# Kernel optimization log

Measured on AMD Instinct MI355X. Metric: run time of the kernel, lower is better.

The kernel has to match this reference:

```python
import jax, jax.numpy as jnp
import numpy as np

D_MODEL = 2048
NUM_EXPERTS = 64
TOP_K = 2
N_TOKENS = 16384


def setup_inputs() -> dict:
    key = jax.random.key(0)
    kx, kw = jax.random.split(key)
    x = jax.random.normal(kx, (N_TOKENS, D_MODEL), dtype=jnp.float32)
    # match nn.Linear default init scale roughly (not bit-exact; math is what matters)
    W = jax.random.normal(kw, (D_MODEL, NUM_EXPERTS), dtype=jnp.float32) * (1.0 / np.sqrt(D_MODEL))
    b = jnp.zeros((NUM_EXPERTS,), dtype=jnp.float32)
    return {"x": x, "W": W, "b": b}


def reference(x, W, b):
    # eval-mode forward (self.training False => no noise)
    logits = jnp.einsum("td,de->te", x, W) + b          # [T, E]
    weights = jax.nn.softmax(logits, axis=-1)             # [T, E]
    topk_weights, topk_indices = jax.lax.top_k(weights, TOP_K)  # [T, k] each
    return topk_weights, topk_indices, weights
```

## Files before the change

kernel.cpp:

```cpp
#include <hip/hip_runtime.h>
#include <math.h>


#define T_TOK 16384
#define DMOD  2048
#define NEXP  64
#define TM    64
#define BK    64
#define NCH   (DMOD / BK)
#define NT    512
#define LDK   72

typedef __attribute__((ext_vector_type(8))) short short8;
typedef __attribute__((ext_vector_type(4))) float f32x4;

__device__ __forceinline__ unsigned short bf16_rne(float f) {
  unsigned int u = __float_as_uint(f);
  unsigned int r = (u + 0x7fffu + ((u >> 16) & 1u)) >> 16;
  return (unsigned short)r;
}
__device__ __forceinline__ float bf16_up(unsigned short h) {
  return __uint_as_float(((unsigned int)h) << 16);
}
__device__ __forceinline__ void split3(float v, unsigned short& h,
                                       unsigned short& m, unsigned short& l) {
  h = bf16_rne(v);
  const float e1 = v - bf16_up(h);
  m = bf16_rne(e1);
  const float e2 = e1 - bf16_up(m);
  l = bf16_rne(e2);
}

__global__ __launch_bounds__(NT, 4) void gating_kernel(
    const float* __restrict__ x, const float* __restrict__ W,
    const float* __restrict__ bias, float* __restrict__ out) {
  __shared__ __align__(16) unsigned short smem[6 * TM * LDK];
  unsigned short* xs_h = smem;
  unsigned short* xs_m = smem + TM * LDK;
  unsigned short* xs_l = smem + 2 * TM * LDK;
  unsigned short* wt_h = smem + 3 * TM * LDK;
  unsigned short* wt_m = smem + 4 * TM * LDK;
  unsigned short* wt_l = smem + 5 * TM * LDK;
  float* lg    = (float*)smem;
  float* red_m = (float*)smem + 4160;
  float* red_s = (float*)smem + 4224;

  const int tid = threadIdx.x;
  const int l   = tid & 63;
  const int w   = tid >> 6;
  const int q   = l >> 4;
  const int c   = l & 15;
  const int t0  = blockIdx.x * TM;

  const int xtok = tid >> 3;
  const int xk0  = (tid & 7) * 8;
  const int wn0  = (tid & 31) * 2;
  const int wk0  = (tid >> 5) * 4;
  const float* xg = x + (size_t)(t0 + xtok) * DMOD + xk0;
  const float* wg = W + (size_t)wk0 * NEXP + wn0;

  const int arow = (w & 3) * 16 + c;
  const int bn0  = (w >> 2) * 32 + c;
  const unsigned short* pa_h = xs_h + arow * LDK + q * 8;
  const unsigned short* pa_m = xs_m + arow * LDK + q * 8;
  const unsigned short* pa_l = xs_l + arow * LDK + q * 8;
  const unsigned short* pb_h = wt_h + bn0 * LDK + q * 8;
  const unsigned short* pb_m = wt_m + bn0 * LDK + q * 8;
  const unsigned short* pb_l = wt_l + bn0 * LDK + q * 8;

  f32x4 acc0 = {0.f, 0.f, 0.f, 0.f};
  f32x4 acc1 = {0.f, 0.f, 0.f, 0.f};

  float4 pxa, pxb;
  float2 pwv[4];
  pxa = *(const float4*)(xg);
  pxb = *(const float4*)(xg + 4);
#pragma unroll
  for (int i = 0; i < 4; ++i) pwv[i] = *(const float2*)(wg + (size_t)i * NEXP);

  for (int k = 0; k < NCH; ++k) {
    {
      float xv[8] = {pxa.x, pxa.y, pxa.z, pxa.w, pxb.x, pxb.y, pxb.z, pxb.w};
      unsigned short h[8], m[8], lo[8];
#pragma unroll
      for (int j = 0; j < 8; ++j) split3(xv[j], h[j], m[j], lo[j]);
      uint4 hp, mp, lp;
      hp.x = (unsigned)h[0] | ((unsigned)h[1] << 16);
      hp.y = (unsigned)h[2] | ((unsigned)h[3] << 16);
      hp.z = (unsigned)h[4] | ((unsigned)h[5] << 16);
      hp.w = (unsigned)h[6] | ((unsigned)h[7] << 16);
      mp.x = (unsigned)m[0] | ((unsigned)m[1] << 16);
      mp.y = (unsigned)m[2] | ((unsigned)m[3] << 16);
      mp.z = (unsigned)m[4] | ((unsigned)m[5] << 16);
      mp.w = (unsigned)m[6] | ((unsigned)m[7] << 16);
      lp.x = (unsigned)lo[0] | ((unsigned)lo[1] << 16);
      lp.y = (unsigned)lo[2] | ((unsigned)lo[3] << 16);
      lp.z = (unsigned)lo[4] | ((unsigned)lo[5] << 16);
      lp.w = (unsigned)lo[6] | ((unsigned)lo[7] << 16);
      *(uint4*)(xs_h + xtok * LDK + xk0) = hp;
      *(uint4*)(xs_m + xtok * LDK + xk0) = mp;
      *(uint4*)(xs_l + xtok * LDK + xk0) = lp;
#pragma unroll
      for (int n = 0; n < 2; ++n) {
        unsigned short wh[4], wm[4], wl[4];
#pragma unroll
        for (int i = 0; i < 4; ++i) {
          const float v = n == 0 ? pwv[i].x : pwv[i].y;
          split3(v, wh[i], wm[i], wl[i]);
        }
        uint2 hp2, mp2, lp2;
        hp2.x = (unsigned)wh[0] | ((unsigned)wh[1] << 16);
        hp2.y = (unsigned)wh[2] | ((unsigned)wh[3] << 16);
        mp2.x = (unsigned)wm[0] | ((unsigned)wm[1] << 16);
        mp2.y = (unsigned)wm[2] | ((unsigned)wm[3] << 16);
        lp2.x = (unsigned)wl[0] | ((unsigned)wl[1] << 16);
        lp2.y = (unsigned)wl[2] | ((unsigned)wl[3] << 16);
        *(uint2*)(wt_h + (wn0 + n) * LDK + wk0) = hp2;
        *(uint2*)(wt_m + (wn0 + n) * LDK + wk0) = mp2;
        *(uint2*)(wt_l + (wn0 + n) * LDK + wk0) = lp2;
      }
    }
    __syncthreads();

    if (k + 1 < NCH) {
      const int kc = (k + 1) * BK;
      pxa = *(const float4*)(xg + kc);
      pxb = *(const float4*)(xg + kc + 4);
#pragma unroll
      for (int i = 0; i < 4; ++i)
        pwv[i] = *(const float2*)(wg + (size_t)(kc + i) * NEXP);
    }

#pragma unroll
    for (int s = 0; s < 2; ++s) {
      const int ko = s * 32;
      const short8 a_h = *(const short8*)(pa_h + ko);
      const short8 a_m = *(const short8*)(pa_m + ko);
      const short8 a_l = *(const short8*)(pa_l + ko);
      const short8 b_h0 = *(const short8*)(pb_h + ko);
      const short8 b_m0 = *(const short8*)(pb_m + ko);
      const short8 b_l0 = *(const short8*)(pb_l + ko);
      const short8 b_h1 = *(const short8*)(pb_h + 16 * LDK + ko);
      const short8 b_m1 = *(const short8*)(pb_m + 16 * LDK + ko);
      const short8 b_l1 = *(const short8*)(pb_l + 16 * LDK + ko);
      acc0 = __builtin_amdgcn_mfma_f32_16x16x32_bf16(a_h, b_h0, acc0, 0, 0, 0);
      acc0 = __builtin_amdgcn_mfma_f32_16x16x32_bf16(a_h, b_m0, acc0, 0, 0, 0);
      acc0 = __builtin_amdgcn_mfma_f32_16x16x32_bf16(a_m, b_h0, acc0, 0, 0, 0);
      acc0 = __builtin_amdgcn_mfma_f32_16x16x32_bf16(a_m, b_m0, acc0, 0, 0, 0);
      acc0 = __builtin_amdgcn_mfma_f32_16x16x32_bf16(a_h, b_l0, acc0, 0, 0, 0);
      acc0 = __builtin_amdgcn_mfma_f32_16x16x32_bf16(a_l, b_h0, acc0, 0, 0, 0);
      acc1 = __builtin_amdgcn_mfma_f32_16x16x32_bf16(a_h, b_h1, acc1, 0, 0, 0);
      acc1 = __builtin_amdgcn_mfma_f32_16x16x32_bf16(a_h, b_m1, acc1, 0, 0, 0);
      acc1 = __builtin_amdgcn_mfma_f32_16x16x32_bf16(a_m, b_h1, acc1, 0, 0, 0);
      acc1 = __builtin_amdgcn_mfma_f32_16x16x32_bf16(a_m, b_m1, acc1, 0, 0, 0);
      acc1 = __builtin_amdgcn_mfma_f32_16x16x32_bf16(a_h, b_l1, acc1, 0, 0, 0);
      acc1 = __builtin_amdgcn_mfma_f32_16x16x32_bf16(a_l, b_h1, acc1, 0, 0, 0);
    }
    __syncthreads();
  }

  {
    const int row0 = (w & 3) * 16 + q * 4;
    const int e0 = (w >> 2) * 32 + c;
    const float bv0 = bias[e0];
    const float bv1 = bias[e0 + 16];
#pragma unroll
    for (int r = 0; r < 4; ++r) {
      lg[(row0 + r) * 65 + e0] = acc0[r] + bv0;
      lg[(row0 + r) * 65 + e0 + 16] = acc1[r] + bv1;
    }
  }
  __syncthreads();

  if (tid < TM) {
    float mx = -INFINITY;
    for (int e = 0; e < NEXP; ++e) mx = fmaxf(mx, lg[tid * 65 + e]);
    float sum = 0.f, b1 = -INFINITY, b2 = -INFINITY;
    int i1 = 0, i2 = 0;
    for (int e = 0; e < NEXP; ++e) {
      const float v = lg[tid * 65 + e];
      sum += expf(v - mx);
      if (v > b1) {
        b2 = b1; i2 = i1; b1 = v; i1 = e;
      } else if (v > b2) {
        b2 = v; i2 = e;
      }
    }
    const float inv = 1.f / sum;
    const int t = t0 + tid;
    out[2 * t + 0] = expf(b1 - mx) * inv;
    out[2 * t + 1] = expf(b2 - mx) * inv;
    out[2 * T_TOK + 2 * t + 0] = (float)i1;
    out[2 * T_TOK + 2 * t + 1] = (float)i2;
    red_m[tid] = mx;
    red_s[tid] = inv;
  }
  __syncthreads();

#pragma unroll
  for (int r = 0; r < (TM * NEXP) / NT; ++r) {
    const int idx = r * NT + tid;
    const int tt = idx >> 6;
    const int e = idx & 63;
    out[4 * T_TOK + (size_t)(t0 + tt) * NEXP + e] =
        expf(lg[tt * 65 + e] - red_m[tt]) * red_s[tt];
  }
}

extern "C" void kernel_launch(void* const* d_in, const int* in_sizes, int n_in,
                              void* d_out, int out_size, void* d_ws, size_t ws_size,
                              hipStream_t stream) {
  const float* x = (const float*)d_in[0];
  const float* W = (const float*)d_in[1];
  const float* b = (const float*)d_in[2];
  float* out = (float*)d_out;
  gating_kernel<<<dim3(T_TOK / TM), dim3(NT), 0, stream>>>(x, W, b, out);
}
```

Baseline: 227.1 us.

## Pre-split W into MFMA fragments and use single-wave blocks without LDS staging

Adds a pre-pass kernel that splits W into bf16 hi/mid/lo parts once, stored in workspace in MFMA fragment order. The gating kernel becomes one wavefront per 16 tokens, reading x straight from global memory into registers and loading B fragments from the prepacked buffer with register double buffering. This removes the per-chunk LDS staging, the barriers and the redundant split of W in every block. In exchange there is an extra launch, heavy register pressure from the prefetch arrays, and W fragments are re-read from L2 by every block. The softmax and top-2 are now split across 4 lanes per token with shuffle reductions.

```diff
diff --git a/kernel.cpp b/kernel.cpp
--- a/kernel.cpp
+++ b/kernel.cpp
@@ -5,14 +5,12 @@
 #define T_TOK 16384
 #define DMOD  2048
 #define NEXP  64
-#define TM    64
-#define BK    64
-#define NCH   (DMOD / BK)
-#define NT    512
-#define LDK   72
+#define NKS   64
 
 typedef __attribute__((ext_vector_type(8))) short short8;
 typedef __attribute__((ext_vector_type(4))) float f32x4;
+
+#define MFMA16 __builtin_amdgcn_mfma_f32_16x16x32_bf16
 
 __device__ __forceinline__ unsigned short bf16_rne(float f) {
   unsigned int u = __float_as_uint(f);
@@ -22,197 +20,202 @@
 __device__ __forceinline__ float bf16_up(unsigned short h) {
   return __uint_as_float(((unsigned int)h) << 16);
 }
-__device__ __forceinline__ void split3(float v, unsigned short& h,
-                                       unsigned short& m, unsigned short& l) {
-  h = bf16_rne(v);
-  const float e1 = v - bf16_up(h);
-  m = bf16_rne(e1);
-  const float e2 = e1 - bf16_up(m);
-  l = bf16_rne(e2);
-}
-
-__global__ __launch_bounds__(NT, 4) void gating_kernel(
-    const float* __restrict__ x, const float* __restrict__ W,
+
+__device__ __forceinline__ void split3_pair(float v0, float v1, unsigned& hp,
+                                            unsigned& mp, unsigned& lp) {
+  const unsigned short h0 = bf16_rne(v0), h1 = bf16_rne(v1);
+  const float e0 = v0 - bf16_up(h0), e1 = v1 - bf16_up(h1);
+  const unsigned short m0 = bf16_rne(e0), m1 = bf16_rne(e1);
+  const float g0 = e0 - bf16_up(m0), g1 = e1 - bf16_up(m1);
+  const unsigned short l0 = bf16_rne(g0), l1 = bf16_rne(g1);
+  hp = (unsigned)h0 | ((unsigned)h1 << 16);
+  mp = (unsigned)m0 | ((unsigned)m1 << 16);
+  lp = (unsigned)l0 | ((unsigned)l1 << 16);
+}
+
+__global__ __launch_bounds__(256) void wconv_kernel(
+    const float* __restrict__ W, unsigned short* __restrict__ wp) {
+  const int tid = blockIdx.x * 256 + threadIdx.x;
+  const int l = tid & 63;
+  const int g = tid >> 6;
+  const int q = l >> 4, c = l & 15;
+  const int ks = g >> 2, nt = g & 3;
+  const int k0 = ks * 32 + q * 8;
+  const int n = nt * 16 + c;
+  float v[8];
+#pragma unroll
+  for (int j = 0; j < 8; ++j) v[j] = W[(size_t)(k0 + j) * NEXP + n];
+  uint4 h, m, lo;
+  split3_pair(v[0], v[1], h.x, m.x, lo.x);
+  split3_pair(v[2], v[3], h.y, m.y, lo.y);
+  split3_pair(v[4], v[5], h.z, m.z, lo.z);
+  split3_pair(v[6], v[7], h.w, m.w, lo.w);
+  unsigned short* base = wp + (size_t)g * 1536 + l * 8;
+  *(uint4*)(base) = h;
+  *(uint4*)(base + 512) = m;
+  *(uint4*)(base + 1024) = lo;
+}
+
+__global__ __launch_bounds__(64) void gating_kernel(
+    const float* __restrict__ x, const unsigned short* __restrict__ wp,
     const float* __restrict__ bias, float* __restrict__ out) {
-  __shared__ __align__(16) unsigned short smem[6 * TM * LDK];
-  unsigned short* xs_h = smem;
-  unsigned short* xs_m = smem + TM * LDK;
-  unsigned short* xs_l = smem + 2 * TM * LDK;
-  unsigned short* wt_h = smem + 3 * TM * LDK;
-  unsigned short* wt_m = smem + 4 * TM * LDK;
-  unsigned short* wt_l = smem + 5 * TM * LDK;
-  float* lg    = (float*)smem;
-  float* red_m = (float*)smem + 4160;
-  float* red_s = (float*)smem + 4224;
-
-  const int tid = threadIdx.x;
-  const int l   = tid & 63;
-  const int w   = tid >> 6;
-  const int q   = l >> 4;
-  const int c   = l & 15;
-  const int t0  = blockIdx.x * TM;
-
-  const int xtok = tid >> 3;
-  const int xk0  = (tid & 7) * 8;
-  const int wn0  = (tid & 31) * 2;
-  const int wk0  = (tid >> 5) * 4;
-  const float* xg = x + (size_t)(t0 + xtok) * DMOD + xk0;
-  const float* wg = W + (size_t)wk0 * NEXP + wn0;
-
-  const int arow = (w & 3) * 16 + c;
-  const int bn0  = (w >> 2) * 32 + c;
-  const unsigned short* pa_h = xs_h + arow * LDK + q * 8;
-  const unsigned short* pa_m = xs_m + arow * LDK + q * 8;
-  const unsigned short* pa_l = xs_l + arow * LDK + q * 8;
-  const unsigned short* pb_h = wt_h + bn0 * LDK + q * 8;
-  const unsigned short* pb_m = wt_m + bn0 * LDK + q * 8;
-  const unsigned short* pb_l = wt_l + bn0 * LDK + q * 8;
-
-  f32x4 acc0 = {0.f, 0.f, 0.f, 0.f};
-  f32x4 acc1 = {0.f, 0.f, 0.f, 0.f};
-
-  float4 pxa, pxb;
-  float2 pwv[4];
-  pxa = *(const float4*)(xg);
-  pxb = *(const float4*)(xg + 4);
-#pragma unroll
-  for (int i = 0; i < 4; ++i) pwv[i] = *(const float2*)(wg + (size_t)i * NEXP);
-
-  for (int k = 0; k < NCH; ++k) {
-    {
-      float xv[8] = {pxa.x, pxa.y, pxa.z, pxa.w, pxb.x, pxb.y, pxb.z, pxb.w};
-      unsigned short h[8], m[8], lo[8];
-#pragma unroll
-      for (int j = 0; j < 8; ++j) split3(xv[j], h[j], m[j], lo[j]);
-      uint4 hp, mp, lp;
-      hp.x = (unsigned)h[0] | ((unsigned)h[1] << 16);
-      hp.y = (unsigned)h[2] | ((unsigned)h[3] << 16);
-      hp.z = (unsigned)h[4] | ((unsigned)h[5] << 16);
-      hp.w = (unsigned)h[6] | ((unsigned)h[7] << 16);
-      mp.x = (unsigned)m[0] | ((unsigned)m[1] << 16);
-      mp.y = (unsigned)m[2] | ((unsigned)m[3] << 16);
-      mp.z = (unsigned)m[4] | ((unsigned)m[5] << 16);
-      mp.w = (unsigned)m[6] | ((unsigned)m[7] << 16);
-      lp.x = (unsigned)lo[0] | ((unsigned)lo[1] << 16);
-      lp.y = (unsigned)lo[2] | ((unsigned)lo[3] << 16);
-      lp.z = (unsigned)lo[4] | ((unsigned)lo[5] << 16);
-      lp.w = (unsigned)lo[6] | ((unsigned)lo[7] << 16);
-      *(uint4*)(xs_h + xtok * LDK + xk0) = hp;
-      *(uint4*)(xs_m + xtok * LDK + xk0) = mp;
-      *(uint4*)(xs_l + xtok * LDK + xk0) = lp;
-#pragma unroll
-      for (int n = 0; n < 2; ++n) {
-        unsigned short wh[4], wm[4], wl[4];
-#pragma unroll
-        for (int i = 0; i < 4; ++i) {
-          const float v = n == 0 ? pwv[i].x : pwv[i].y;
-          split3(v, wh[i], wm[i], wl[i]);
-        }
-        uint2 hp2, mp2, lp2;
-        hp2.x = (unsigned)wh[0] | ((unsigned)wh[1] << 16);
-        hp2.y = (unsigned)wh[2] | ((unsigned)wh[3] << 16);
-        mp2.x = (unsigned)wm[0] | ((unsigned)wm[1] << 16);
-        mp2.y = (unsigned)wm[2] | ((unsigned)wm[3] << 16);
-        lp2.x = (unsigned)wl[0] | ((unsigned)wl[1] << 16);
-        lp2.y = (unsigned)wl[2] | ((unsigned)wl[3] << 16);
-        *(uint2*)(wt_h + (wn0 + n) * LDK + wk0) = hp2;
-        *(uint2*)(wt_m + (wn0 + n) * LDK + wk0) = mp2;
-        *(uint2*)(wt_l + (wn0 + n) * LDK + wk0) = lp2;
-      }
-    }
-    __syncthreads();
-
-    if (k + 1 < NCH) {
-      const int kc = (k + 1) * BK;
-      pxa = *(const float4*)(xg + kc);
-      pxb = *(const float4*)(xg + kc + 4);
-#pragma unroll
-      for (int i = 0; i < 4; ++i)
-        pwv[i] = *(const float2*)(wg + (size_t)(kc + i) * NEXP);
-    }
-
-#pragma unroll
-    for (int s = 0; s < 2; ++s) {
-      const int ko = s * 32;
-      const short8 a_h = *(const short8*)(pa_h + ko);
-      const short8 a_m = *(const short8*)(pa_m + ko);
-      const short8 a_l = *(const short8*)(pa_l + ko);
-      const short8 b_h0 = *(const short8*)(pb_h + ko);
-      const short8 b_m0 = *(const short8*)(pb_m + ko);
-      const short8 b_l0 = *(const short8*)(pb_l + ko);
-      const short8 b_h1 = *(const short8*)(pb_h + 16 * LDK + ko);
-      const short8 b_m1 = *(const short8*)(pb_m + 16 * LDK + ko);
-      const short8 b_l1 = *(const short8*)(pb_l + 16 * LDK + ko);
-      acc0 = __builtin_amdgcn_mfma_f32_16x16x32_bf16(a_h, b_h0, acc0, 0, 0, 0);
-      acc0 = __builtin_amdgcn_mfma_f32_16x16x32_bf16(a_h, b_m0, acc0, 0, 0, 0);
-      acc0 = __builtin_amdgcn_mfma_f32_16x16x32_bf16(a_m, b_h0, acc0, 0, 0, 0);
-      acc0 = __builtin_amdgcn_mfma_f32_16x16x32_bf16(a_m, b_m0, acc0, 0, 0, 0);
-      acc0 = __builtin_amdgcn_mfma_f32_16x16x32_bf16(a_h, b_l0, acc0, 0, 0, 0);
-      acc0 = __builtin_amdgcn_mfma_f32_16x16x32_bf16(a_l, b_h0, acc0, 0, 0, 0);
-      acc1 = __builtin_amdgcn_mfma_f32_16x16x32_bf16(a_h, b_h1, acc1, 0, 0, 0);
-      acc1 = __builtin_amdgcn_mfma_f32_16x16x32_bf16(a_h, b_m1, acc1, 0, 0, 0);
-      acc1 = __builtin_amdgcn_mfma_f32_16x16x32_bf16(a_m, b_h1, acc1, 0, 0, 0);
-      acc1 = __builtin_amdgcn_mfma_f32_16x16x32_bf16(a_m, b_m1, acc1, 0, 0, 0);
-      acc1 = __builtin_amdgcn_mfma_f32_16x16x32_bf16(a_h, b_l1, acc1, 0, 0, 0);
-      acc1 = __builtin_amdgcn_mfma_f32_16x16x32_bf16(a_l, b_h1, acc1, 0, 0, 0);
-    }
-    __syncthreads();
-  }
+  __shared__ float lg[16 * 65];
+  __shared__ float red_m[16];
+  __shared__ float red_s[16];
+
+  const int l = threadIdx.x;
+  const int q = l >> 4, c = l & 15;
+  const int t0 = blockIdx.x * 16;
+
+  const float* xg = x + (size_t)(t0 + c) * DMOD + q * 8;
+  const unsigned short* wl = wp + l * 8;
+
+  float bv[4];
+#pragma unroll
+  for (int nt = 0; nt < 4; ++nt) bv[nt] = bias[nt * 16 + c];
+
+  f32x4 acc[4];
+#pragma unroll
+  for (int nt = 0; nt < 4; ++nt) acc[nt] = (f32x4){0.f, 0.f, 0.f, 0.f};
+
+  float4 xr[4][2];
+  short8 bb[2][12];
+
+#pragma unroll
+  for (int i = 0; i < 4; ++i) {
+    xr[i][0] = *(const float4*)(xg + i * 32);
+    xr[i][1] = *(const float4*)(xg + i * 32 + 4);
+  }
+#pragma unroll
+  for (int i = 0; i < 12; ++i) {
+    bb[0][i] = *(const short8*)(wl + (size_t)i * 512);
+    bb[1][i] = *(const short8*)(wl + (size_t)(12 + i) * 512);
+  }
+
+  for (int blk = 0; blk < 16; ++blk) {
+#pragma unroll
+    for (int u = 0; u < 4; ++u) {
+      const int ks = blk * 4 + u;
+      short8 ah, am, al;
+      {
+        uint4 h, m, lo;
+        split3_pair(xr[u][0].x, xr[u][0].y, h.x, m.x, lo.x);
+        split3_pair(xr[u][0].z, xr[u][0].w, h.y, m.y, lo.y);
+        split3_pair(xr[u][1].x, xr[u][1].y, h.z, m.z, lo.z);
+        split3_pair(xr[u][1].z, xr[u][1].w, h.w, m.w, lo.w);
+        ah = *(short8*)&h;
+        am = *(short8*)&m;
+        al = *(short8*)&lo;
+      }
+      {
+        const int kn = (ks + 4 < NKS) ? ks + 4 : NKS - 1;
+        xr[u][0] = *(const float4*)(xg + kn * 32);
+        xr[u][1] = *(const float4*)(xg + kn * 32 + 4);
+      }
+      const int pb = u & 1;
+#pragma unroll
+      for (int nt = 0; nt < 4; ++nt) {
+        const short8 bh = bb[pb][nt * 3 + 0];
+        const short8 bm = bb[pb][nt * 3 + 1];
+        const short8 bl = bb[pb][nt * 3 + 2];
+        acc[nt] = MFMA16(ah, bh, acc[nt], 0, 0, 0);
+        acc[nt] = MFMA16(ah, bm, acc[nt], 0, 0, 0);
+        acc[nt] = MFMA16(am, bh, acc[nt], 0, 0, 0);
+        acc[nt] = MFMA16(am, bm, acc[nt], 0, 0, 0);
+        acc[nt] = MFMA16(ah, bl, acc[nt], 0, 0, 0);
+        acc[nt] = MFMA16(al, bh, acc[nt], 0, 0, 0);
+      }
+      {
+        const int kn = (ks + 2 < NKS) ? ks + 2 : NKS - 1;
+        const unsigned short* src = wl + (size_t)kn * 6144;
+#pragma unroll
+        for (int i = 0; i < 12; ++i)
+          bb[pb][i] = *(const short8*)(src + (size_t)i * 512);
+      }
+    }
+  }
+
+#pragma unroll
+  for (int nt = 0; nt < 4; ++nt)
+#pragma unroll
+    for (int r = 0; r < 4; ++r)
+      lg[(q * 4 + r) * 65 + nt * 16 + c] = acc[nt][r] + bv[nt];
+  __syncthreads();
 
   {
-    const int row0 = (w & 3) * 16 + q * 4;
-    const int e0 = (w >> 2) * 32 + c;
-    const float bv0 = bias[e0];
-    const float bv1 = bias[e0 + 16];
-#pragma unroll
-    for (int r = 0; r < 4; ++r) {
-      lg[(row0 + r) * 65 + e0] = acc0[r] + bv0;
-      lg[(row0 + r) * 65 + e0 + 16] = acc1[r] + bv1;
-    }
-  }
-  __syncthreads();
-
-  if (tid < TM) {
+    const int row = l >> 2;
+    const int s = l & 3;
+    const float* lr = lg + row * 65 + s * 16;
     float mx = -INFINITY;
-    for (int e = 0; e < NEXP; ++e) mx = fmaxf(mx, lg[tid * 65 + e]);
+#pragma unroll
+    for (int e = 0; e < 16; ++e) mx = fmaxf(mx, lr[e]);
+    mx = fmaxf(mx, __shfl_xor(mx, 1));
+    mx = fmaxf(mx, __shfl_xor(mx, 2));
     float sum = 0.f, b1 = -INFINITY, b2 = -INFINITY;
     int i1 = 0, i2 = 0;
-    for (int e = 0; e < NEXP; ++e) {
-      const float v = lg[tid * 65 + e];
+#pragma unroll
+    for (int e = 0; e < 16; ++e) {
+      const float v = lr[e];
       sum += expf(v - mx);
+      const int idx = s * 16 + e;
       if (v > b1) {
-        b2 = b1; i2 = i1; b1 = v; i1 = e;
+        b2 = b1; i2 = i1; b1 = v; i1 = idx;
       } else if (v > b2) {
-        b2 = v; i2 = e;
-      }
-    }
-    const float inv = 1.f / sum;
-    const int t = t0 + tid;
-    out[2 * t + 0] = expf(b1 - mx) * inv;
-    out[2 * t + 1] = expf(b2 - mx) * inv;
-    out[2 * T_TOK + 2 * t + 0] = (float)i1;
-    out[2 * T_TOK + 2 * t + 1] = (float)i2;
-    red_m[tid] = mx;
-    red_s[tid] = inv;
+        b2 = v; i2 = idx;
+      }
+    }
+#pragma unroll
+    for (int msk = 1; msk <= 2; msk <<= 1) {
+      sum += __shfl_xor(sum, msk);
+      const float ob1 = __shfl_xor(b1, msk);
+      const int oi1 = __shfl_xor(i1, msk);
+      const float ob2 = __shfl_xor(b2, msk);
+      const int oi2 = __shfl_xor(i2, msk);
+      float n1, n2;
+      int j1, j2;
+      const bool aFirst = (b1 > ob1) || (b1 == ob1 && i1 < oi1);
+      if (aFirst) {
+        n1 = b1; j1 = i1;
+        const bool t = (b2 > ob1) || (b2 == ob1 && i2 < oi1);
+        n2 = t ? b2 : ob1; j2 = t ? i2 : oi1;
+      } else {
+        n1 = ob1; j1 = oi1;
+        const bool t = (ob2 > b1) || (ob2 == b1 && oi2 < i1);
+        n2 = t ? ob2 : b1; j2 = t ? oi2 : i1;
+      }
+      b1 = n1; i1 = j1; b2 = n2; i2 = j2;
+    }
+    if (s == 0) {
+      const float inv = 1.f / sum;
+      const int t = t0 + row;
+      float2 wv, iv;
+      wv.x = expf(b1 - mx) * inv;
+      wv.y = expf(b2 - mx) * inv;
+      iv.x = (float)i1;
+      iv.y = (float)i2;
+      *(float2*)(out + 2 * t) = wv;
+      *(float2*)(out + 2 * T_TOK + 2 * t) = iv;
+      red_m[row] = mx;
+      red_s[row] = inv;
+    }
   }
   __syncthreads();
 
 #pragma unroll
-  for (int r = 0; r < (TM * NEXP) / NT; ++r) {
-    const int idx = r * NT + tid;
-    const int tt = idx >> 6;
-    const int e = idx & 63;
-    out[4 * T_TOK + (size_t)(t0 + tt) * NEXP + e] =
-        expf(lg[tt * 65 + e] - red_m[tt]) * red_s[tt];
+  for (int it = 0; it < 16; ++it) {
+    out[4 * T_TOK + (size_t)(t0 + it) * NEXP + l] =
+        expf(lg[it * 65 + l] - red_m[it]) * red_s[it];
   }
 }
 
 extern "C" void kernel_launch(void* const* d_in, const int* in_sizes, int n_in,
-                              void* d_out, int out_size, void* d_ws, size_t ws_size,
-                              hipStream_t stream) {
+                              void* d_out, int out_size, void* d_ws,
+                              size_t ws_size, hipStream_t stream) {
   const float* x = (const float*)d_in[0];
   const float* W = (const float*)d_in[1];
   const float* b = (const float*)d_in[2];
   float* out = (float*)d_out;
-  gating_kernel<<<dim3(T_TOK / TM), dim3(NT), 0, stream>>>(x, W, b, out);
-}
+  unsigned short* wp = (unsigned short*)d_ws;
+  wconv_kernel<<<dim3(64), dim3(256), 0, stream>>>(W, wp);
+  gating_kernel<<<dim3(T_TOK / 16), dim3(64), 0, stream>>>(x, wp, b, out);
+}
```

Measured after the change: 232.6 us. 2.4% more time.
